# Optimization experiments

Hardware: AMD Instinct MI355X
Metric: run time of the kernel (lower is better)

## Reference

```python
import jax, jax.numpy as jnp
import numpy as np

HIDDEN = 2048
INTER = 5632
N_EXPERTS = 8
TOP_K = 2


def setup_inputs() -> dict:
    key = jax.random.key(0)
    ks = jax.random.split(key, 6)
    x = jax.random.normal(ks[0], (4, 2048, HIDDEN), dtype=jnp.float32)
    router_w = jax.random.normal(ks[1], (N_EXPERTS, HIDDEN), dtype=jnp.float32) * 0.02
    router_b = jnp.zeros((N_EXPERTS,), dtype=jnp.float32)
    Wg = jax.random.normal(ks[2], (N_EXPERTS, INTER, HIDDEN), dtype=jnp.float32) * 0.02
    Wu = jax.random.normal(ks[3], (N_EXPERTS, INTER, HIDDEN), dtype=jnp.float32) * 0.02
    Wd = jax.random.normal(ks[4], (N_EXPERTS, HIDDEN, INTER), dtype=jnp.float32) * 0.02
    return {"x": x, "router_w": router_w, "router_b": router_b, "Wg": Wg, "Wu": Wu, "Wd": Wd}


def reference(x, router_w, router_b, Wg, Wu, Wd):
    batch_shape = x.shape[:-1]
    xf = x.reshape(-1, HIDDEN)  # [T, H]
    T = xf.shape[0]

    # Router: softmax -> top-k -> renormalize (matches torch forward)
    logits = xf @ router_w.T + router_b            # [T, E]
    probs = jax.nn.softmax(logits, axis=-1)
    w, idx = jax.lax.top_k(probs, TOP_K)           # [T, K]
    w = w / jnp.sum(w, axis=-1, keepdims=True)

    # Dense combine weights [T, E]: zero where expert not selected.
    combine = jnp.zeros((T, N_EXPERTS), dtype=xf.dtype)
    combine = combine.at[jnp.arange(T)[:, None], idx].set(w)

    # Weighted sum of SwiGLU expert outputs (loop over fixed small E).
    out = jnp.zeros_like(xf)
    for e in range(N_EXPERTS):
        g = jax.nn.silu(xf @ Wg[e].T)              # [T, I]
        u = xf @ Wu[e].T                           # [T, I]
        h = (g * u) @ Wd[e].T                      # [T, H]
        out = out + combine[:, e:e + 1] * h
    return out.reshape(*batch_shape, HIDDEN)
```

## Files before the change

kernel.cpp:

```cpp
#include <hip/hip_runtime.h>
#include <stdint.h>

#define HID 2048
#define ITR 5632
#define NE 8
#define TT 8192
#define BM 128
#define BN 128
#define BK 64
#define MT1 64
#define NT1 44
#define NT2 16

typedef __attribute__((ext_vector_type(4))) float f4;
typedef __attribute__((ext_vector_type(8))) short s8v;
typedef __attribute__((ext_vector_type(4))) float acc4;
typedef __attribute__((ext_vector_type(4))) unsigned short u4v;
typedef __attribute__((ext_vector_type(8))) unsigned short u8v;

__device__ __forceinline__ unsigned short f2bf(float f) {
    union { float f; uint32_t u; } v; v.f = f;
    uint32_t u = v.u;
    return (unsigned short)((u + 0x7FFFu + ((u >> 16) & 1u)) >> 16);
}

__device__ __forceinline__ void gload16(const unsigned short* g, unsigned short* l) {
    __builtin_amdgcn_global_load_lds(
        (const __attribute__((address_space(1))) unsigned int*)g,
        (__attribute__((address_space(3))) unsigned int*)l, 16, 0, 0);
}

__global__ __launch_bounds__(256) void k_cvt(const float* __restrict__ src,
                                             unsigned short* __restrict__ dst) {
    size_t i = ((size_t)blockIdx.x * 256 + threadIdx.x) * 8;
    f4 a = *(const f4*)(src + i);
    f4 b = *(const f4*)(src + i + 4);
    u8v o;
    o[0]=f2bf(a.x); o[1]=f2bf(a.y); o[2]=f2bf(a.z); o[3]=f2bf(a.w);
    o[4]=f2bf(b.x); o[5]=f2bf(b.y); o[6]=f2bf(b.z); o[7]=f2bf(b.w);
    *(u8v*)(dst + i) = o;
}

#define WBLK 45056
__global__ __launch_bounds__(256) void k_cvtW(const float* __restrict__ a,
                                              const float* __restrict__ b,
                                              const float* __restrict__ c,
                                              unsigned short* __restrict__ oa,
                                              unsigned short* __restrict__ ob,
                                              unsigned short* __restrict__ oc) {
    int bb = blockIdx.x;
    const float* s; unsigned short* d;
    if (bb < WBLK)            { s = a; d = oa; }
    else if (bb < 2 * WBLK)   { s = b; d = ob; bb -= WBLK; }
    else                      { s = c; d = oc; bb -= 2 * WBLK; }
    size_t i = ((size_t)bb * 256 + threadIdx.x) * 8;
    f4 va = *(const f4*)(s + i);
    f4 vb = *(const f4*)(s + i + 4);
    u8v o;
    o[0]=f2bf(va.x); o[1]=f2bf(va.y); o[2]=f2bf(va.z); o[3]=f2bf(va.w);
    o[4]=f2bf(vb.x); o[5]=f2bf(vb.y); o[6]=f2bf(vb.z); o[7]=f2bf(vb.w);
    *(u8v*)(d + i) = o;
}

__global__ __launch_bounds__(256) void k_router(const float* __restrict__ x,
                                                const float* __restrict__ rw,
                                                const float* __restrict__ rb,
                                                int* __restrict__ cnt,
                                                int* __restrict__ tokL,
                                                int* __restrict__ slotL,
                                                float* __restrict__ gateL) {
    int lane = threadIdx.x & 63;
    int wv = threadIdx.x >> 6;
    int t = blockIdx.x * 4 + wv;
    const float* xr = x + (size_t)t * HID;
    float acc[NE];
    #pragma unroll
    for (int e = 0; e < NE; ++e) acc[e] = 0.f;
    #pragma unroll
    for (int i = 0; i < 8; ++i) {
        f4 xv = *(const f4*)(xr + i * 256 + lane * 4);
        #pragma unroll
        for (int e = 0; e < NE; ++e) {
            f4 wv4 = *(const f4*)(rw + e * HID + i * 256 + lane * 4);
            acc[e] += xv.x * wv4.x + xv.y * wv4.y + xv.z * wv4.z + xv.w * wv4.w;
        }
    }
    #pragma unroll
    for (int off = 32; off; off >>= 1)
        #pragma unroll
        for (int e = 0; e < NE; ++e) acc[e] += __shfl_xor(acc[e], off, 64);
    if (lane == 0) {
        float lg[NE];
        #pragma unroll
        for (int e = 0; e < NE; ++e) lg[e] = acc[e] + rb[e];
        int i1 = 0;
        #pragma unroll
        for (int e = 1; e < NE; ++e) if (lg[e] > lg[i1]) i1 = e;
        int i2 = -1;
        #pragma unroll
        for (int e = 0; e < NE; ++e) {
            if (e == i1) continue;
            if (i2 < 0 || lg[e] > lg[i2]) i2 = e;
        }
        float ex = __expf(lg[i2] - lg[i1]);
        float w1 = 1.f / (1.f + ex);
        float w2 = ex / (1.f + ex);
        int p = atomicAdd(&cnt[i1], 1);
        tokL[i1 * TT + p] = t; slotL[i1 * TT + p] = t * 2;     gateL[i1 * TT + p] = w1;
        p = atomicAdd(&cnt[i2], 1);
        tokL[i2 * TT + p] = t; slotL[i2 * TT + p] = t * 2 + 1; gateL[i2 * TT + p] = w2;
    }
}


__global__ __launch_bounds__(256, 2) void k_gemm1b(const unsigned short* __restrict__ xb,
                                                   const unsigned short* __restrict__ WgB,
                                                   const unsigned short* __restrict__ WuB,
                                                   const int* __restrict__ cnt,
                                                   const int* __restrict__ tokL,
                                                   const int* __restrict__ slotL,
                                                   unsigned short* __restrict__ Hb) {
    int bx = blockIdx.x;
    int xcd = bx & 7;
    int j = bx >> 3;
    int g = xcd * NT1 + (j >> 6);
    int mt = j & 63;
    int e = g / NT1;
    int nt = g % NT1;
    int M = cnt[e];
    int m0 = mt * BM;
    if (m0 >= M) return;
    int n0 = nt * BN;

    __shared__ __align__(16) unsigned short lA[BM * BK];
    __shared__ __align__(16) unsigned short lBg[BN * BK];
    __shared__ __align__(16) unsigned short lBu[BN * BK];
    __shared__ int sTok[BM];
    __shared__ int sSlot[BM];

    int tid = threadIdx.x;
    if (tid < BM) {
        int m = m0 + tid;
        int mc = m < M ? m : M - 1;
        sTok[tid] = tokL[e * TT + mc];
        sSlot[tid] = slotL[e * TT + mc];
    }
    __syncthreads();

    int wv = tid >> 6, lane = tid & 63;
    int subrow = lane >> 3;
    int colE = ((lane & 7) ^ subrow) * 8;

    const unsigned short* aSrc[4];
    const unsigned short* gSrc[4];
    const unsigned short* uSrc[4];
    #pragma unroll
    for (int i = 0; i < 4; ++i) {
        int row = (i * 4 + wv) * 8 + subrow;
        aSrc[i] = xb + (size_t)sTok[row] * HID + colE;
        gSrc[i] = WgB + ((size_t)e * ITR + n0 + row) * HID + colE;
        uSrc[i] = WuB + ((size_t)e * ITR + n0 + row) * HID + colE;
    }

    int wm = (wv >> 1) * 64, wn = (wv & 1) * 64;
    int lr = lane & 15, lk = (lane >> 4) * 8;

    acc4 zero4 = {0.f, 0.f, 0.f, 0.f};
    acc4 ag[4][4], au[4][4];
    #pragma unroll
    for (int mi = 0; mi < 4; ++mi)
        #pragma unroll
        for (int ni = 0; ni < 4; ++ni) { ag[mi][ni] = zero4; au[mi][ni] = zero4; }

    for (int k0 = 0; k0 < HID; k0 += BK) {
        if (k0) __syncthreads();
        #pragma unroll
        for (int i = 0; i < 4; ++i) {
            gload16(aSrc[i] + k0, lA  + (i * 4 + wv) * 512);
            gload16(gSrc[i] + k0, lBg + (i * 4 + wv) * 512);
            gload16(uSrc[i] + k0, lBu + (i * 4 + wv) * 512);
        }
        __syncthreads();
        #pragma unroll
        for (int kk = 0; kk < BK; kk += 32) {
            s8v af[4], gf[4], uf[4];
            #pragma unroll
            for (int i = 0; i < 4; ++i) {
                int rowA = wm + i * 16 + lr;
                af[i] = *(const s8v*)((char*)lA + ((rowA * 128 + (kk + lk) * 2) ^ ((rowA & 7) << 4)));
                int rowB = wn + i * 16 + lr;
                int bb = (rowB * 128 + (kk + lk) * 2) ^ ((rowB & 7) << 4);
                gf[i] = *(const s8v*)((char*)lBg + bb);
                uf[i] = *(const s8v*)((char*)lBu + bb);
            }
            #pragma unroll
            for (int mi = 0; mi < 4; ++mi)
                #pragma unroll
                for (int ni = 0; ni < 4; ++ni) {
                    ag[mi][ni] = __builtin_amdgcn_mfma_f32_16x16x32_bf16(af[mi], gf[ni], ag[mi][ni], 0, 0, 0);
                    au[mi][ni] = __builtin_amdgcn_mfma_f32_16x16x32_bf16(af[mi], uf[ni], au[mi][ni], 0, 0, 0);
                }
        }
    }
    #pragma unroll
    for (int mi = 0; mi < 4; ++mi) {
        #pragma unroll
        for (int j2 = 0; j2 < 4; ++j2) {
            int m = wm + mi * 16 + (lane >> 4) * 4 + j2;
            if (m0 + m < M) {
                size_t rowOff = (size_t)sSlot[m] * ITR + n0 + wn + lr;
                #pragma unroll
                for (int ni = 0; ni < 4; ++ni) {
                    float g2 = ag[mi][ni][j2], u = au[mi][ni][j2];
                    float h = g2 * (1.f / (1.f + __expf(-g2))) * u;
                    Hb[rowOff + ni * 16] = f2bf(h);
                }
            }
        }
    }
}

__global__ __launch_bounds__(256, 3) void k_gemm2b(const unsigned short* __restrict__ Hb,
                                                   const unsigned short* __restrict__ WdB,
                                                   const int* __restrict__ cnt,
                                                   const int* __restrict__ tokL,
                                                   const int* __restrict__ slotL,
                                                   const float* __restrict__ gateL,
                                                   float* __restrict__ out) {
    int bx = blockIdx.x;
    int xcd = bx & 7;
    int j = bx >> 3;
    int g = xcd * NT2 + (j >> 6);
    int mt = j & 63;
    int e = g / NT2;
    int nt = g % NT2;
    int M = cnt[e];
    int m0 = mt * BM;
    if (m0 >= M) return;
    int n0 = nt * BN;

    __shared__ __align__(16) unsigned short lA[BM * BK];
    __shared__ __align__(16) unsigned short lB[BN * BK];
    __shared__ int sTok[BM];
    __shared__ int sSlot[BM];
    __shared__ float sGate[BM];

    int tid = threadIdx.x;
    if (tid < BM) {
        int m = m0 + tid;
        int mc = m < M ? m : M - 1;
        sTok[tid] = tokL[e * TT + mc];
        sSlot[tid] = slotL[e * TT + mc];
        sGate[tid] = gateL[e * TT + mc];
    }
    __syncthreads();

    int wv = tid >> 6, lane = tid & 63;
    int subrow = lane >> 3;
    int colE = ((lane & 7) ^ subrow) * 8;

    const unsigned short* aSrc[4];
    const unsigned short* bSrc[4];
    #pragma unroll
    for (int i = 0; i < 4; ++i) {
        int row = (i * 4 + wv) * 8 + subrow;
        aSrc[i] = Hb + (size_t)sSlot[row] * ITR + colE;
        bSrc[i] = WdB + ((size_t)e * HID + n0 + row) * ITR + colE;
    }

    int wm = (wv >> 1) * 64, wn = (wv & 1) * 64;
    int lr = lane & 15, lk = (lane >> 4) * 8;

    acc4 zero4 = {0.f, 0.f, 0.f, 0.f};
    acc4 a4[4][4];
    #pragma unroll
    for (int mi = 0; mi < 4; ++mi)
        #pragma unroll
        for (int ni = 0; ni < 4; ++ni) a4[mi][ni] = zero4;

    for (int k0 = 0; k0 < ITR; k0 += BK) {
        if (k0) __syncthreads();
        #pragma unroll
        for (int i = 0; i < 4; ++i) {
            gload16(aSrc[i] + k0, lA + (i * 4 + wv) * 512);
            gload16(bSrc[i] + k0, lB + (i * 4 + wv) * 512);
        }
        __syncthreads();
        #pragma unroll
        for (int kk = 0; kk < BK; kk += 32) {
            s8v af[4], bf[4];
            #pragma unroll
            for (int i = 0; i < 4; ++i) {
                int rowA = wm + i * 16 + lr;
                af[i] = *(const s8v*)((char*)lA + ((rowA * 128 + (kk + lk) * 2) ^ ((rowA & 7) << 4)));
                int rowB = wn + i * 16 + lr;
                bf[i] = *(const s8v*)((char*)lB + ((rowB * 128 + (kk + lk) * 2) ^ ((rowB & 7) << 4)));
            }
            #pragma unroll
            for (int mi = 0; mi < 4; ++mi)
                #pragma unroll
                for (int ni = 0; ni < 4; ++ni)
                    a4[mi][ni] = __builtin_amdgcn_mfma_f32_16x16x32_bf16(af[mi], bf[ni], a4[mi][ni], 0, 0, 0);
        }
    }
    #pragma unroll
    for (int mi = 0; mi < 4; ++mi) {
        #pragma unroll
        for (int j2 = 0; j2 < 4; ++j2) {
            int m = wm + mi * 16 + (lane >> 4) * 4 + j2;
            if (m0 + m < M) {
                int t = sTok[m];
                float w = sGate[m];
                float* orow = out + (size_t)t * HID + n0 + wn + lr;
                #pragma unroll
                for (int ni = 0; ni < 4; ++ni)
                    atomicAdd(orow + ni * 16, w * a4[mi][ni][j2]);
            }
        }
    }
}


__global__ __launch_bounds__(256) void k_gemm1(const unsigned short* __restrict__ xb,
                                               const float* __restrict__ Wg,
                                               const float* __restrict__ Wu,
                                               const int* __restrict__ cnt,
                                               const int* __restrict__ tokL,
                                               const int* __restrict__ slotL,
                                               unsigned short* __restrict__ Hb) {
    int bx = blockIdx.x;
    int e = bx / (MT1 * NT1);
    int r = bx % (MT1 * NT1);
    int mt = r / NT1, nt = r % NT1;
    int M = cnt[e];
    int m0 = mt * BM;
    if (m0 >= M) return;
    int n0 = nt * BN;

    __shared__ __align__(16) unsigned short lA[BM * BK];
    __shared__ __align__(16) unsigned short lBg[BN * BK];
    __shared__ __align__(16) unsigned short lBu[BN * BK];
    __shared__ int sTok[BM];
    __shared__ int sSlot[BM];

    int tid = threadIdx.x;
    if (tid < BM) {
        int m = m0 + tid;
        int mc = m < M ? m : M - 1;
        sTok[tid] = tokL[e * TT + mc];
        sSlot[tid] = slotL[e * TT + mc];
    }
    __syncthreads();

    int ar = tid >> 3, ac = tid & 7;
    const unsigned short* aP[4];
    #pragma unroll
    for (int i = 0; i < 4; ++i)
        aP[i] = xb + (size_t)sTok[ar + 32 * i] * HID + ac * 8;

    int br = tid >> 4, bc = tid & 15;
    const float* gB = Wg + ((size_t)e * ITR + n0) * HID + bc * 4;
    const float* uB = Wu + ((size_t)e * ITR + n0) * HID + bc * 4;

    int wv = tid >> 6, lane = tid & 63;
    int wm = (wv >> 1) * 64, wn = (wv & 1) * 64;
    int lr = lane & 15, lk = (lane >> 4) * 8;

    acc4 zero4 = {0.f, 0.f, 0.f, 0.f};
    acc4 ag[4][4], au[4][4];
    #pragma unroll
    for (int mi = 0; mi < 4; ++mi)
        #pragma unroll
        for (int ni = 0; ni < 4; ++ni) { ag[mi][ni] = zero4; au[mi][ni] = zero4; }

    for (int k0 = 0; k0 < HID; k0 += BK) {
        if (k0) __syncthreads();
        #pragma unroll
        for (int i = 0; i < 4; ++i) {
            int row = ar + 32 * i;
            s8v v = *(const s8v*)(aP[i] + k0);
            int byt = (row * 128 + ac * 16) ^ ((row & 7) << 4);
            *(s8v*)((char*)lA + byt) = v;
        }
        #pragma unroll
        for (int i = 0; i < 8; ++i) {
            int row = br + 16 * i;
            f4 vg = *(const f4*)(gB + (size_t)row * HID + k0);
            f4 vu = *(const f4*)(uB + (size_t)row * HID + k0);
            u4v og = { f2bf(vg.x), f2bf(vg.y), f2bf(vg.z), f2bf(vg.w) };
            u4v ou = { f2bf(vu.x), f2bf(vu.y), f2bf(vu.z), f2bf(vu.w) };
            int byt = (row * 128 + bc * 8) ^ ((row & 7) << 4);
            *(u4v*)((char*)lBg + byt) = og;
            *(u4v*)((char*)lBu + byt) = ou;
        }
        __syncthreads();
        #pragma unroll
        for (int kk = 0; kk < BK; kk += 32) {
            s8v af[4], gf[4], uf[4];
            #pragma unroll
            for (int i = 0; i < 4; ++i) {
                int rowA = wm + i * 16 + lr;
                af[i] = *(const s8v*)((char*)lA + ((rowA * 128 + (kk + lk) * 2) ^ ((rowA & 7) << 4)));
                int rowB = wn + i * 16 + lr;
                int bb = (rowB * 128 + (kk + lk) * 2) ^ ((rowB & 7) << 4);
                gf[i] = *(const s8v*)((char*)lBg + bb);
                uf[i] = *(const s8v*)((char*)lBu + bb);
            }
            #pragma unroll
            for (int mi = 0; mi < 4; ++mi)
                #pragma unroll
                for (int ni = 0; ni < 4; ++ni) {
                    ag[mi][ni] = __builtin_amdgcn_mfma_f32_16x16x32_bf16(af[mi], gf[ni], ag[mi][ni], 0, 0, 0);
                    au[mi][ni] = __builtin_amdgcn_mfma_f32_16x16x32_bf16(af[mi], uf[ni], au[mi][ni], 0, 0, 0);
                }
        }
    }
    #pragma unroll
    for (int mi = 0; mi < 4; ++mi) {
        #pragma unroll
        for (int j = 0; j < 4; ++j) {
            int m = wm + mi * 16 + (lane >> 4) * 4 + j;
            if (m0 + m < M) {
                size_t rowOff = (size_t)sSlot[m] * ITR + n0 + wn + lr;
                #pragma unroll
                for (int ni = 0; ni < 4; ++ni) {
                    float g = ag[mi][ni][j], u = au[mi][ni][j];
                    float h = g * (1.f / (1.f + __expf(-g))) * u;
                    Hb[rowOff + ni * 16] = f2bf(h);
                }
            }
        }
    }
}

__global__ __launch_bounds__(256) void k_gemm2(const unsigned short* __restrict__ Hb,
                                               const float* __restrict__ Wd,
                                               const int* __restrict__ cnt,
                                               const int* __restrict__ tokL,
                                               const int* __restrict__ slotL,
                                               const float* __restrict__ gateL,
                                               float* __restrict__ out) {
    int bx = blockIdx.x;
    int e = bx / (MT1 * NT2);
    int r = bx % (MT1 * NT2);
    int mt = r / NT2, nt = r % NT2;
    int M = cnt[e];
    int m0 = mt * BM;
    if (m0 >= M) return;
    int n0 = nt * BN;

    __shared__ __align__(16) unsigned short lA[BM * BK];
    __shared__ __align__(16) unsigned short lB[BN * BK];
    __shared__ int sTok[BM];
    __shared__ int sSlot[BM];
    __shared__ float sGate[BM];

    int tid = threadIdx.x;
    if (tid < BM) {
        int m = m0 + tid;
        int mc = m < M ? m : M - 1;
        sTok[tid] = tokL[e * TT + mc];
        sSlot[tid] = slotL[e * TT + mc];
        sGate[tid] = gateL[e * TT + mc];
    }
    __syncthreads();

    int ar = tid >> 3, ac = tid & 7;
    const unsigned short* aP[4];
    #pragma unroll
    for (int i = 0; i < 4; ++i)
        aP[i] = Hb + (size_t)sSlot[ar + 32 * i] * ITR + ac * 8;

    int br = tid >> 4, bc = tid & 15;
    const float* dB = Wd + ((size_t)e * HID + n0) * ITR + bc * 4;

    int wv = tid >> 6, lane = tid & 63;
    int wm = (wv >> 1) * 64, wn = (wv & 1) * 64;
    int lr = lane & 15, lk = (lane >> 4) * 8;

    acc4 zero4 = {0.f, 0.f, 0.f, 0.f};
    acc4 a4[4][4];
    #pragma unroll
    for (int mi = 0; mi < 4; ++mi)
        #pragma unroll
        for (int ni = 0; ni < 4; ++ni) a4[mi][ni] = zero4;

    for (int k0 = 0; k0 < ITR; k0 += BK) {
        if (k0) __syncthreads();
        #pragma unroll
        for (int i = 0; i < 4; ++i) {
            int row = ar + 32 * i;
            s8v v = *(const s8v*)(aP[i] + k0);
            int byt = (row * 128 + ac * 16) ^ ((row & 7) << 4);
            *(s8v*)((char*)lA + byt) = v;
        }
        #pragma unroll
        for (int i = 0; i < 8; ++i) {
            int row = br + 16 * i;
            f4 vd = *(const f4*)(dB + (size_t)row * ITR + k0);
            u4v od = { f2bf(vd.x), f2bf(vd.y), f2bf(vd.z), f2bf(vd.w) };
            int byt = (row * 128 + bc * 8) ^ ((row & 7) << 4);
            *(u4v*)((char*)lB + byt) = od;
        }
        __syncthreads();
        #pragma unroll
        for (int kk = 0; kk < BK; kk += 32) {
            s8v af[4], bf[4];
            #pragma unroll
            for (int i = 0; i < 4; ++i) {
                int rowA = wm + i * 16 + lr;
                af[i] = *(const s8v*)((char*)lA + ((rowA * 128 + (kk + lk) * 2) ^ ((rowA & 7) << 4)));
                int rowB = wn + i * 16 + lr;
                bf[i] = *(const s8v*)((char*)lB + ((rowB * 128 + (kk + lk) * 2) ^ ((rowB & 7) << 4)));
            }
            #pragma unroll
            for (int mi = 0; mi < 4; ++mi)
                #pragma unroll
                for (int ni = 0; ni < 4; ++ni)
                    a4[mi][ni] = __builtin_amdgcn_mfma_f32_16x16x32_bf16(af[mi], bf[ni], a4[mi][ni], 0, 0, 0);
        }
    }
    #pragma unroll
    for (int mi = 0; mi < 4; ++mi) {
        #pragma unroll
        for (int j = 0; j < 4; ++j) {
            int m = wm + mi * 16 + (lane >> 4) * 4 + j;
            if (m0 + m < M) {
                int t = sTok[m];
                float w = sGate[m];
                float* orow = out + (size_t)t * HID + n0 + wn + lr;
                #pragma unroll
                for (int ni = 0; ni < 4; ++ni)
                    atomicAdd(orow + ni * 16, w * a4[mi][ni][j]);
            }
        }
    }
}

extern "C" void kernel_launch(void* const* d_in, const int* in_sizes, int n_in,
                              void* d_out, int out_size, void* d_ws, size_t ws_size,
                              hipStream_t stream) {
    const float* x  = (const float*)d_in[0];
    const float* rw = (const float*)d_in[1];
    const float* rb = (const float*)d_in[2];
    const float* Wg = (const float*)d_in[3];
    const float* Wu = (const float*)d_in[4];
    const float* Wd = (const float*)d_in[5];
    float* out = (float*)d_out;
    char* ws = (char*)d_ws;

    const size_t OFF_XB   = 0;
    const size_t OFF_HB   = 33554432ull;
    const size_t OFF_TOK  = 218103808ull;
    const size_t OFF_SLOT = 218365952ull;
    const size_t OFF_GATE = 218628096ull;
    const size_t OFF_CNT  = 218890240ull;
    const size_t OFF_WG   = 218891264ull;
    const size_t OFF_WU   = 403440640ull;
    const size_t OFF_WD   = 587990016ull;
    const size_t NEED     = 772539392ull;

    unsigned short* xb   = (unsigned short*)(ws + OFF_XB);
    unsigned short* Hb   = (unsigned short*)(ws + OFF_HB);
    int*   tokL  = (int*)(ws + OFF_TOK);
    int*   slotL = (int*)(ws + OFF_SLOT);
    float* gateL = (float*)(ws + OFF_GATE);
    int*   cnt   = (int*)(ws + OFF_CNT);

    hipMemsetAsync(cnt, 0, NE * sizeof(int), stream);
    hipMemsetAsync(out, 0, (size_t)out_size * sizeof(float), stream);
    k_cvt<<<8192, 256, 0, stream>>>(x, xb);
    k_router<<<2048, 256, 0, stream>>>(x, rw, rb, cnt, tokL, slotL, gateL);

    if (ws_size >= NEED) {
        unsigned short* WgB = (unsigned short*)(ws + OFF_WG);
        unsigned short* WuB = (unsigned short*)(ws + OFF_WU);
        unsigned short* WdB = (unsigned short*)(ws + OFF_WD);
        k_cvtW<<<3 * WBLK, 256, 0, stream>>>(Wg, Wu, Wd, WgB, WuB, WdB);
        k_gemm1b<<<NE * MT1 * NT1, 256, 0, stream>>>(xb, WgB, WuB, cnt, tokL, slotL, Hb);
        k_gemm2b<<<NE * MT1 * NT2, 256, 0, stream>>>(Hb, WdB, cnt, tokL, slotL, gateL, out);
    } else {
        k_gemm1<<<NE * MT1 * NT1, 256, 0, stream>>>(xb, Wg, Wu, cnt, tokL, slotL, Hb);
        k_gemm2<<<NE * MT1 * NT2, 256, 0, stream>>>(Hb, Wd, cnt, tokL, slotL, gateL, out);
    }
}
```

Measured before the change: 1.909 ms.

## Replace grouped GEMM kernels with 512-thread, 4-stage pipelined, larger-tile versions

Replaces both expert GEMM kernels with 512-thread variants that use 256-row tiles and a 4-deep ring of 32-wide K slices in LDS. Direct global-to-LDS loads for later stages are issued while MFMAs run on the current stage, with manual waitcnt/barrier control and raised priority around the MFMA block. The larger tiles raise reuse of weight and activation loads, and the ring buffer hides global latency behind compute. The trade-off is higher LDS use and register pressure. The XCD-aware block remapping is also dropped, and expert-row imbalance may leave more 256-row tiles partly empty.

```diff
diff --git a/kernel.cpp b/kernel.cpp
--- a/kernel.cpp
+++ b/kernel.cpp
@@ -5,18 +5,13 @@
 #define ITR 5632
 #define NE 8
 #define TT 8192
-#define BM 128
-#define BN 128
-#define BK 64
-#define MT1 64
-#define NT1 44
-#define NT2 16
 
 typedef __attribute__((ext_vector_type(4))) float f4;
 typedef __attribute__((ext_vector_type(8))) short s8v;
 typedef __attribute__((ext_vector_type(4))) float acc4;
 typedef __attribute__((ext_vector_type(4))) unsigned short u4v;
 typedef __attribute__((ext_vector_type(8))) unsigned short u8v;
+typedef unsigned short ushort_t;
 
 __device__ __forceinline__ unsigned short f2bf(float f) {
     union { float f; uint32_t u; } v; v.f = f;
@@ -28,6 +23,10 @@
     __builtin_amdgcn_global_load_lds(
         (const __attribute__((address_space(1))) unsigned int*)g,
         (__attribute__((address_space(3))) unsigned int*)l, 16, 0, 0);
+}
+
+__device__ __forceinline__ int lby(int row, int s) {
+    return row * 64 + ((s ^ ((row >> 1) & 3)) * 16);
 }
 
 __global__ __launch_bounds__(256) void k_cvt(const float* __restrict__ src,
@@ -113,20 +112,263 @@
 }
 
 
-__global__ __launch_bounds__(256, 2) void k_gemm1b(const unsigned short* __restrict__ xb,
-                                                   const unsigned short* __restrict__ WgB,
-                                                   const unsigned short* __restrict__ WuB,
-                                                   const int* __restrict__ cnt,
-                                                   const int* __restrict__ tokL,
-                                                   const int* __restrict__ slotL,
-                                                   unsigned short* __restrict__ Hb) {
+__global__ __launch_bounds__(512, 2) void k_g1p(const unsigned short* __restrict__ xb,
+                                                const unsigned short* __restrict__ WgB,
+                                                const unsigned short* __restrict__ WuB,
+                                                const int* __restrict__ cnt,
+                                                const int* __restrict__ tokL,
+                                                const int* __restrict__ slotL,
+                                                unsigned short* __restrict__ Hb) {
     int bx = blockIdx.x;
-    int xcd = bx & 7;
-    int j = bx >> 3;
-    int g = xcd * NT1 + (j >> 6);
-    int mt = j & 63;
-    int e = g / NT1;
-    int nt = g % NT1;
+    int e = bx / (32 * 44);
+    int r = bx % (32 * 44);
+    int mt = r / 44, nt = r % 44;
+    int M = cnt[e];
+    int m0 = mt * 256;
+    if (m0 >= M) return;
+    int n0 = nt * 128;
+
+    __shared__ __align__(16) unsigned short lds[65536];
+    __shared__ int sTok[256];
+    __shared__ int sSlot[256];
+
+    int tid = threadIdx.x;
+    if (tid < 256) {
+        int m = m0 + tid;
+        int mc = m < M ? m : M - 1;
+        sTok[tid]  = tokL[e * TT + mc];
+        sSlot[tid] = slotL[e * TT + mc];
+    }
+    __syncthreads();
+
+    int wv = tid >> 6, lane = tid & 63;
+    int lrow = lane >> 2;
+    int slog = (lane & 3) ^ ((lane >> 3) & 3);
+
+    const unsigned short* aS0 = xb + (size_t)sTok[(2 * wv) * 16 + lrow] * HID + slog * 8;
+    const unsigned short* aS1 = xb + (size_t)sTok[(2 * wv + 1) * 16 + lrow] * HID + slog * 8;
+    const unsigned short* gS  = WgB + ((size_t)e * ITR + n0 + wv * 16 + lrow) * HID + slog * 8;
+    const unsigned short* uS  = WuB + ((size_t)e * ITR + n0 + wv * 16 + lrow) * HID + slog * 8;
+
+    unsigned short* ldsA = lds;
+    unsigned short* ldsG = lds + 32768;
+    unsigned short* ldsU = lds + 49152;
+
+    auto STAGE = [&](int reg, int kh) {
+        int ko = kh * 32;
+        gload16(aS0 + ko, ldsA + reg * 8192 + (2 * wv) * 512);
+        gload16(aS1 + ko, ldsA + reg * 8192 + (2 * wv + 1) * 512);
+        gload16(gS + ko,  ldsG + reg * 4096 + wv * 512);
+        gload16(uS + ko,  ldsU + reg * 4096 + wv * 512);
+    };
+
+    int wr = wv >> 2, wc = wv & 3;
+    int lr = lane & 15, ls = lane >> 4;
+
+    int aOff[8], gOff[2], uOff[2];
+    #pragma unroll
+    for (int mi = 0; mi < 8; ++mi) aOff[mi] = lby(wr * 128 + mi * 16 + lr, ls);
+    #pragma unroll
+    for (int ni = 0; ni < 2; ++ni) {
+        gOff[ni] = 65536 + lby(wc * 32 + ni * 16 + lr, ls);
+        uOff[ni] = 98304 + lby(wc * 32 + ni * 16 + lr, ls);
+    }
+
+    acc4 zero4 = {0.f, 0.f, 0.f, 0.f};
+    acc4 ag[8][2], au[8][2];
+    #pragma unroll
+    for (int mi = 0; mi < 8; ++mi)
+        #pragma unroll
+        for (int ni = 0; ni < 2; ++ni) { ag[mi][ni] = zero4; au[mi][ni] = zero4; }
+
+    STAGE(0, 0); STAGE(1, 1); STAGE(2, 2); STAGE(3, 3);
+    asm volatile("s_waitcnt vmcnt(12)" ::: "memory");
+    __builtin_amdgcn_s_barrier();
+
+    #pragma unroll 4
+    for (int h = 0; h < 64; ++h) {
+        int reg = h & 3;
+        const char* baseA = (const char*)lds + reg * 16384;
+        const char* baseB = (const char*)lds + reg * 8192;
+        s8v af[8], gf[2], uf[2];
+        #pragma unroll
+        for (int mi = 0; mi < 8; ++mi) af[mi] = *(const s8v*)(baseA + aOff[mi]);
+        #pragma unroll
+        for (int ni = 0; ni < 2; ++ni) {
+            gf[ni] = *(const s8v*)(baseB + gOff[ni]);
+            uf[ni] = *(const s8v*)(baseB + uOff[ni]);
+        }
+        asm volatile("s_waitcnt lgkmcnt(0)" ::: "memory");
+        __builtin_amdgcn_sched_barrier(0);
+        __builtin_amdgcn_s_barrier();
+        __builtin_amdgcn_sched_barrier(0);
+        int kh = h + 4 < 64 ? h + 4 : 63;
+        STAGE(reg, kh);
+        __builtin_amdgcn_s_setprio(1);
+        #pragma unroll
+        for (int mi = 0; mi < 8; ++mi)
+            #pragma unroll
+            for (int ni = 0; ni < 2; ++ni) {
+                ag[mi][ni] = __builtin_amdgcn_mfma_f32_16x16x32_bf16(af[mi], gf[ni], ag[mi][ni], 0, 0, 0);
+                au[mi][ni] = __builtin_amdgcn_mfma_f32_16x16x32_bf16(af[mi], uf[ni], au[mi][ni], 0, 0, 0);
+            }
+        __builtin_amdgcn_s_setprio(0);
+        asm volatile("s_waitcnt vmcnt(12)" ::: "memory");
+        __builtin_amdgcn_s_barrier();
+    }
+    asm volatile("s_waitcnt vmcnt(0)" ::: "memory");
+
+    #pragma unroll
+    for (int mi = 0; mi < 8; ++mi) {
+        #pragma unroll
+        for (int j = 0; j < 4; ++j) {
+            int m = wr * 128 + mi * 16 + ls * 4 + j;
+            if (m0 + m < M) {
+                size_t rowOff = (size_t)sSlot[m] * ITR + n0 + wc * 32 + lr;
+                #pragma unroll
+                for (int ni = 0; ni < 2; ++ni) {
+                    float g = ag[mi][ni][j], u = au[mi][ni][j];
+                    float h2 = g * (1.f / (1.f + __expf(-g))) * u;
+                    Hb[rowOff + ni * 16] = f2bf(h2);
+                }
+            }
+        }
+    }
+}
+
+__global__ __launch_bounds__(512, 2) void k_g2p(const unsigned short* __restrict__ Hb,
+                                                const unsigned short* __restrict__ WdB,
+                                                const int* __restrict__ cnt,
+                                                const int* __restrict__ tokL,
+                                                const int* __restrict__ slotL,
+                                                const float* __restrict__ gateL,
+                                                float* __restrict__ out) {
+    int bx = blockIdx.x;
+    int e = bx / (32 * 8);
+    int r = bx % (32 * 8);
+    int mt = r / 8, nt = r % 8;
+    int M = cnt[e];
+    int m0 = mt * 256;
+    if (m0 >= M) return;
+    int n0 = nt * 256;
+
+    __shared__ __align__(16) unsigned short lds[65536];
+    __shared__ int sTok[256];
+    __shared__ int sSlot[256];
+    __shared__ float sGate[256];
+
+    int tid = threadIdx.x;
+    if (tid < 256) {
+        int m = m0 + tid;
+        int mc = m < M ? m : M - 1;
+        sTok[tid]  = tokL[e * TT + mc];
+        sSlot[tid] = slotL[e * TT + mc];
+        sGate[tid] = gateL[e * TT + mc];
+    }
+    __syncthreads();
+
+    int wv = tid >> 6, lane = tid & 63;
+    int lrow = lane >> 2;
+    int slog = (lane & 3) ^ ((lane >> 3) & 3);
+
+    const unsigned short* aS0 = Hb + (size_t)sSlot[(2 * wv) * 16 + lrow] * ITR + slog * 8;
+    const unsigned short* aS1 = Hb + (size_t)sSlot[(2 * wv + 1) * 16 + lrow] * ITR + slog * 8;
+    const unsigned short* bS0 = WdB + ((size_t)e * HID + n0 + (2 * wv) * 16 + lrow) * ITR + slog * 8;
+    const unsigned short* bS1 = WdB + ((size_t)e * HID + n0 + (2 * wv + 1) * 16 + lrow) * ITR + slog * 8;
+
+    unsigned short* ldsA = lds;
+    unsigned short* ldsB = lds + 32768;
+
+    auto STAGE = [&](int reg, int kh) {
+        int ko = kh * 32;
+        gload16(aS0 + ko, ldsA + reg * 8192 + (2 * wv) * 512);
+        gload16(aS1 + ko, ldsA + reg * 8192 + (2 * wv + 1) * 512);
+        gload16(bS0 + ko, ldsB + reg * 8192 + (2 * wv) * 512);
+        gload16(bS1 + ko, ldsB + reg * 8192 + (2 * wv + 1) * 512);
+    };
+
+    int wr = wv >> 2, wc = wv & 3;
+    int lr = lane & 15, ls = lane >> 4;
+
+    int aOff[8], bOff[4];
+    #pragma unroll
+    for (int mi = 0; mi < 8; ++mi) aOff[mi] = lby(wr * 128 + mi * 16 + lr, ls);
+    #pragma unroll
+    for (int ni = 0; ni < 4; ++ni) bOff[ni] = 65536 + lby(wc * 64 + ni * 16 + lr, ls);
+
+    acc4 zero4 = {0.f, 0.f, 0.f, 0.f};
+    acc4 a4[8][4];
+    #pragma unroll
+    for (int mi = 0; mi < 8; ++mi)
+        #pragma unroll
+        for (int ni = 0; ni < 4; ++ni) a4[mi][ni] = zero4;
+
+    STAGE(0, 0); STAGE(1, 1); STAGE(2, 2); STAGE(3, 3);
+    asm volatile("s_waitcnt vmcnt(12)" ::: "memory");
+    __builtin_amdgcn_s_barrier();
+
+    #pragma unroll 4
+    for (int h = 0; h < 176; ++h) {
+        int reg = h & 3;
+        const char* base = (const char*)lds + reg * 16384;
+        s8v af[8], bf[4];
+        #pragma unroll
+        for (int mi = 0; mi < 8; ++mi) af[mi] = *(const s8v*)(base + aOff[mi]);
+        #pragma unroll
+        for (int ni = 0; ni < 4; ++ni) bf[ni] = *(const s8v*)(base + bOff[ni]);
+        asm volatile("s_waitcnt lgkmcnt(0)" ::: "memory");
+        __builtin_amdgcn_sched_barrier(0);
+        __builtin_amdgcn_s_barrier();
+        __builtin_amdgcn_sched_barrier(0);
+        int kh = h + 4 < 176 ? h + 4 : 175;
+        STAGE(reg, kh);
+        __builtin_amdgcn_s_setprio(1);
+        #pragma unroll
+        for (int mi = 0; mi < 8; ++mi)
+            #pragma unroll
+            for (int ni = 0; ni < 4; ++ni)
+                a4[mi][ni] = __builtin_amdgcn_mfma_f32_16x16x32_bf16(af[mi], bf[ni], a4[mi][ni], 0, 0, 0);
+        __builtin_amdgcn_s_setprio(0);
+        asm volatile("s_waitcnt vmcnt(12)" ::: "memory");
+        __builtin_amdgcn_s_barrier();
+    }
+    asm volatile("s_waitcnt vmcnt(0)" ::: "memory");
+
+    #pragma unroll
+    for (int mi = 0; mi < 8; ++mi) {
+        #pragma unroll
+        for (int j = 0; j < 4; ++j) {
+            int m = wr * 128 + mi * 16 + ls * 4 + j;
+            if (m0 + m < M) {
+                int t = sTok[m];
+                float w = sGate[m];
+                float* orow = out + (size_t)t * HID + n0 + wc * 64 + lr;
+                #pragma unroll
+                for (int ni = 0; ni < 4; ++ni)
+                    atomicAdd(orow + ni * 16, w * a4[mi][ni][j]);
+            }
+        }
+    }
+}
+
+#define BM 128
+#define BN 128
+#define BK 64
+#define MT1 64
+#define NT1 44
+#define NT2 16
+
+__global__ __launch_bounds__(256) void k_gemm1(const unsigned short* __restrict__ xb,
+                                               const float* __restrict__ Wg,
+                                               const float* __restrict__ Wu,
+                                               const int* __restrict__ cnt,
+                                               const int* __restrict__ tokL,
+                                               const int* __restrict__ slotL,
+                                               unsigned short* __restrict__ Hb) {
+    int bx = blockIdx.x;
+    int e = bx / (MT1 * NT1);
+    int r = bx % (MT1 * NT1);
+    int mt = r / NT1, nt = r % NT1;
     int M = cnt[e];
     int m0 = mt * BM;
     if (m0 >= M) return;
@@ -147,21 +389,17 @@
     }
     __syncthreads();
 
+    int ar = tid >> 3, ac = tid & 7;
+    const unsigned short* aP[4];
+    #pragma unroll
+    for (int i = 0; i < 4; ++i)
+        aP[i] = xb + (size_t)sTok[ar + 32 * i] * HID + ac * 8;
+
+    int br = tid >> 4, bc = tid & 15;
+    const float* gB = Wg + ((size_t)e * ITR + n0) * HID + bc * 4;
+    const float* uB = Wu + ((size_t)e * ITR + n0) * HID + bc * 4;
+
     int wv = tid >> 6, lane = tid & 63;
-    int subrow = lane >> 3;
-    int colE = ((lane & 7) ^ subrow) * 8;
-
-    const unsigned short* aSrc[4];
-    const unsigned short* gSrc[4];
-    const unsigned short* uSrc[4];
-    #pragma unroll
-    for (int i = 0; i < 4; ++i) {
-        int row = (i * 4 + wv) * 8 + subrow;
-        aSrc[i] = xb + (size_t)sTok[row] * HID + colE;
-        gSrc[i] = WgB + ((size_t)e * ITR + n0 + row) * HID + colE;
-        uSrc[i] = WuB + ((size_t)e * ITR + n0 + row) * HID + colE;
-    }
-
     int wm = (wv >> 1) * 64, wn = (wv & 1) * 64;
     int lr = lane & 15, lk = (lane >> 4) * 8;
 
@@ -176,9 +414,21 @@
         if (k0) __syncthreads();
         #pragma unroll
         for (int i = 0; i < 4; ++i) {
-            gload16(aSrc[i] + k0, lA  + (i * 4 + wv) * 512);
-            gload16(gSrc[i] + k0, lBg + (i * 4 + wv) * 512);
-            gload16(uSrc[i] + k0, lBu + (i * 4 + wv) * 512);
+            int row = ar + 32 * i;
+            s8v v = *(const s8v*)(aP[i] + k0);
+            int byt = (row * 128 + ac * 16) ^ ((row & 7) << 4);
+            *(s8v*)((char*)lA + byt) = v;
+        }
+        #pragma unroll
+        for (int i = 0; i < 8; ++i) {
+            int row = br + 16 * i;
+            f4 vg = *(const f4*)(gB + (size_t)row * HID + k0);
+            f4 vu = *(const f4*)(uB + (size_t)row * HID + k0);
+            u4v og = { f2bf(vg.x), f2bf(vg.y), f2bf(vg.z), f2bf(vg.w) };
+            u4v ou = { f2bf(vu.x), f2bf(vu.y), f2bf(vu.z), f2bf(vu.w) };
+            int byt = (row * 128 + bc * 8) ^ ((row & 7) << 4);
+            *(u4v*)((char*)lBg + byt) = og;
+            *(u4v*)((char*)lBu + byt) = ou;
         }
         __syncthreads();
         #pragma unroll
@@ -205,219 +455,6 @@
     #pragma unroll
     for (int mi = 0; mi < 4; ++mi) {
         #pragma unroll
-        for (int j2 = 0; j2 < 4; ++j2) {
-            int m = wm + mi * 16 + (lane >> 4) * 4 + j2;
-            if (m0 + m < M) {
-                size_t rowOff = (size_t)sSlot[m] * ITR + n0 + wn + lr;
-                #pragma unroll
-                for (int ni = 0; ni < 4; ++ni) {
-                    float g2 = ag[mi][ni][j2], u = au[mi][ni][j2];
-                    float h = g2 * (1.f / (1.f + __expf(-g2))) * u;
-                    Hb[rowOff + ni * 16] = f2bf(h);
-                }
-            }
-        }
-    }
-}
-
-__global__ __launch_bounds__(256, 3) void k_gemm2b(const unsigned short* __restrict__ Hb,
-                                                   const unsigned short* __restrict__ WdB,
-                                                   const int* __restrict__ cnt,
-                                                   const int* __restrict__ tokL,
-                                                   const int* __restrict__ slotL,
-                                                   const float* __restrict__ gateL,
-                                                   float* __restrict__ out) {
-    int bx = blockIdx.x;
-    int xcd = bx & 7;
-    int j = bx >> 3;
-    int g = xcd * NT2 + (j >> 6);
-    int mt = j & 63;
-    int e = g / NT2;
-    int nt = g % NT2;
-    int M = cnt[e];
-    int m0 = mt * BM;
-    if (m0 >= M) return;
-    int n0 = nt * BN;
-
-    __shared__ __align__(16) unsigned short lA[BM * BK];
-    __shared__ __align__(16) unsigned short lB[BN * BK];
-    __shared__ int sTok[BM];
-    __shared__ int sSlot[BM];
-    __shared__ float sGate[BM];
-
-    int tid = threadIdx.x;
-    if (tid < BM) {
-        int m = m0 + tid;
-        int mc = m < M ? m : M - 1;
-        sTok[tid] = tokL[e * TT + mc];
-        sSlot[tid] = slotL[e * TT + mc];
-        sGate[tid] = gateL[e * TT + mc];
-    }
-    __syncthreads();
-
-    int wv = tid >> 6, lane = tid & 63;
-    int subrow = lane >> 3;
-    int colE = ((lane & 7) ^ subrow) * 8;
-
-    const unsigned short* aSrc[4];
-    const unsigned short* bSrc[4];
-    #pragma unroll
-    for (int i = 0; i < 4; ++i) {
-        int row = (i * 4 + wv) * 8 + subrow;
-        aSrc[i] = Hb + (size_t)sSlot[row] * ITR + colE;
-        bSrc[i] = WdB + ((size_t)e * HID + n0 + row) * ITR + colE;
-    }
-
-    int wm = (wv >> 1) * 64, wn = (wv & 1) * 64;
-    int lr = lane & 15, lk = (lane >> 4) * 8;
-
-    acc4 zero4 = {0.f, 0.f, 0.f, 0.f};
-    acc4 a4[4][4];
-    #pragma unroll
-    for (int mi = 0; mi < 4; ++mi)
-        #pragma unroll
-        for (int ni = 0; ni < 4; ++ni) a4[mi][ni] = zero4;
-
-    for (int k0 = 0; k0 < ITR; k0 += BK) {
-        if (k0) __syncthreads();
-        #pragma unroll
-        for (int i = 0; i < 4; ++i) {
-            gload16(aSrc[i] + k0, lA + (i * 4 + wv) * 512);
-            gload16(bSrc[i] + k0, lB + (i * 4 + wv) * 512);
-        }
-        __syncthreads();
-        #pragma unroll
-        for (int kk = 0; kk < BK; kk += 32) {
-            s8v af[4], bf[4];
-            #pragma unroll
-            for (int i = 0; i < 4; ++i) {
-                int rowA = wm + i * 16 + lr;
-                af[i] = *(const s8v*)((char*)lA + ((rowA * 128 + (kk + lk) * 2) ^ ((rowA & 7) << 4)));
-                int rowB = wn + i * 16 + lr;
-                bf[i] = *(const s8v*)((char*)lB + ((rowB * 128 + (kk + lk) * 2) ^ ((rowB & 7) << 4)));
-            }
-            #pragma unroll
-            for (int mi = 0; mi < 4; ++mi)
-                #pragma unroll
-                for (int ni = 0; ni < 4; ++ni)
-                    a4[mi][ni] = __builtin_amdgcn_mfma_f32_16x16x32_bf16(af[mi], bf[ni], a4[mi][ni], 0, 0, 0);
-        }
-    }
-    #pragma unroll
-    for (int mi = 0; mi < 4; ++mi) {
-        #pragma unroll
-        for (int j2 = 0; j2 < 4; ++j2) {
-            int m = wm + mi * 16 + (lane >> 4) * 4 + j2;
-            if (m0 + m < M) {
-                int t = sTok[m];
-                float w = sGate[m];
-                float* orow = out + (size_t)t * HID + n0 + wn + lr;
-                #pragma unroll
-                for (int ni = 0; ni < 4; ++ni)
-                    atomicAdd(orow + ni * 16, w * a4[mi][ni][j2]);
-            }
-        }
-    }
-}
-
-
-__global__ __launch_bounds__(256) void k_gemm1(const unsigned short* __restrict__ xb,
-                                               const float* __restrict__ Wg,
-                                               const float* __restrict__ Wu,
-                                               const int* __restrict__ cnt,
-                                               const int* __restrict__ tokL,
-                                               const int* __restrict__ slotL,
-                                               unsigned short* __restrict__ Hb) {
-    int bx = blockIdx.x;
-    int e = bx / (MT1 * NT1);
-    int r = bx % (MT1 * NT1);
-    int mt = r / NT1, nt = r % NT1;
-    int M = cnt[e];
-    int m0 = mt * BM;
-    if (m0 >= M) return;
-    int n0 = nt * BN;
-
-    __shared__ __align__(16) unsigned short lA[BM * BK];
-    __shared__ __align__(16) unsigned short lBg[BN * BK];
-    __shared__ __align__(16) unsigned short lBu[BN * BK];
-    __shared__ int sTok[BM];
-    __shared__ int sSlot[BM];
-
-    int tid = threadIdx.x;
-    if (tid < BM) {
-        int m = m0 + tid;
-        int mc = m < M ? m : M - 1;
-        sTok[tid] = tokL[e * TT + mc];
-        sSlot[tid] = slotL[e * TT + mc];
-    }
-    __syncthreads();
-
-    int ar = tid >> 3, ac = tid & 7;
-    const unsigned short* aP[4];
-    #pragma unroll
-    for (int i = 0; i < 4; ++i)
-        aP[i] = xb + (size_t)sTok[ar + 32 * i] * HID + ac * 8;
-
-    int br = tid >> 4, bc = tid & 15;
-    const float* gB = Wg + ((size_t)e * ITR + n0) * HID + bc * 4;
-    const float* uB = Wu + ((size_t)e * ITR + n0) * HID + bc * 4;
-
-    int wv = tid >> 6, lane = tid & 63;
-    int wm = (wv >> 1) * 64, wn = (wv & 1) * 64;
-    int lr = lane & 15, lk = (lane >> 4) * 8;
-
-    acc4 zero4 = {0.f, 0.f, 0.f, 0.f};
-    acc4 ag[4][4], au[4][4];
-    #pragma unroll
-    for (int mi = 0; mi < 4; ++mi)
-        #pragma unroll
-        for (int ni = 0; ni < 4; ++ni) { ag[mi][ni] = zero4; au[mi][ni] = zero4; }
-
-    for (int k0 = 0; k0 < HID; k0 += BK) {
-        if (k0) __syncthreads();
-        #pragma unroll
-        for (int i = 0; i < 4; ++i) {
-            int row = ar + 32 * i;
-            s8v v = *(const s8v*)(aP[i] + k0);
-            int byt = (row * 128 + ac * 16) ^ ((row & 7) << 4);
-            *(s8v*)((char*)lA + byt) = v;
-        }
-        #pragma unroll
-        for (int i = 0; i < 8; ++i) {
-            int row = br + 16 * i;
-            f4 vg = *(const f4*)(gB + (size_t)row * HID + k0);
-            f4 vu = *(const f4*)(uB + (size_t)row * HID + k0);
-            u4v og = { f2bf(vg.x), f2bf(vg.y), f2bf(vg.z), f2bf(vg.w) };
-            u4v ou = { f2bf(vu.x), f2bf(vu.y), f2bf(vu.z), f2bf(vu.w) };
-            int byt = (row * 128 + bc * 8) ^ ((row & 7) << 4);
-            *(u4v*)((char*)lBg + byt) = og;
-            *(u4v*)((char*)lBu + byt) = ou;
-        }
-        __syncthreads();
-        #pragma unroll
-        for (int kk = 0; kk < BK; kk += 32) {
-            s8v af[4], gf[4], uf[4];
-            #pragma unroll
-            for (int i = 0; i < 4; ++i) {
-                int rowA = wm + i * 16 + lr;
-                af[i] = *(const s8v*)((char*)lA + ((rowA * 128 + (kk + lk) * 2) ^ ((rowA & 7) << 4)));
-                int rowB = wn + i * 16 + lr;
-                int bb = (rowB * 128 + (kk + lk) * 2) ^ ((rowB & 7) << 4);
-                gf[i] = *(const s8v*)((char*)lBg + bb);
-                uf[i] = *(const s8v*)((char*)lBu + bb);
-            }
-            #pragma unroll
-            for (int mi = 0; mi < 4; ++mi)
-                #pragma unroll
-                for (int ni = 0; ni < 4; ++ni) {
-                    ag[mi][ni] = __builtin_amdgcn_mfma_f32_16x16x32_bf16(af[mi], gf[ni], ag[mi][ni], 0, 0, 0);
-                    au[mi][ni] = __builtin_amdgcn_mfma_f32_16x16x32_bf16(af[mi], uf[ni], au[mi][ni], 0, 0, 0);
-                }
-        }
-    }
-    #pragma unroll
-    for (int mi = 0; mi < 4; ++mi) {
-        #pragma unroll
         for (int j = 0; j < 4; ++j) {
             int m = wm + mi * 16 + (lane >> 4) * 4 + j;
             if (m0 + m < M) {
@@ -577,8 +614,8 @@
         unsigned short* WuB = (unsigned short*)(ws + OFF_WU);
         unsigned short* WdB = (unsigned short*)(ws + OFF_WD);
         k_cvtW<<<3 * WBLK, 256, 0, stream>>>(Wg, Wu, Wd, WgB, WuB, WdB);
-        k_gemm1b<<<NE * MT1 * NT1, 256, 0, stream>>>(xb, WgB, WuB, cnt, tokL, slotL, Hb);
-        k_gemm2b<<<NE * MT1 * NT2, 256, 0, stream>>>(Hb, WdB, cnt, tokL, slotL, gateL, out);
+        k_g1p<<<NE * 32 * 44, 512, 0, stream>>>(xb, WgB, WuB, cnt, tokL, slotL, Hb);
+        k_g2p<<<NE * 32 * 8, 512, 0, stream>>>(Hb, WdB, cnt, tokL, slotL, gateL, out);
     } else {
         k_gemm1<<<NE * MT1 * NT1, 256, 0, stream>>>(xb, Wg, Wu, cnt, tokL, slotL, Hb);
         k_gemm2<<<NE * MT1 * NT2, 256, 0, stream>>>(Hb, Wd, cnt, tokL, slotL, gateL, out);
```

Result: no change. 1.938 ms (+1.5%).

## Fuse x bf16 conversion into router and drop XCD block swizzle

Applied to the files above, without the earlier changes.

Merges the standalone fp32-to-bf16 conversion of x into the router kernel, so x is read once and one launch is removed. Also replaces the XCD-aware block index remapping in both expert GEMMs with a plain linear expert/m-tile/n-tile decomposition. The fusion cuts memory traffic. Dropping the swizzle risks worse L2 locality, because blocks sharing weight tiles now spread across chiplets.

```diff
diff --git a/kernel.cpp b/kernel.cpp
--- a/kernel.cpp
+++ b/kernel.cpp
@@ -30,15 +30,60 @@
         (__attribute__((address_space(3))) unsigned int*)l, 16, 0, 0);
 }
 
-__global__ __launch_bounds__(256) void k_cvt(const float* __restrict__ src,
-                                             unsigned short* __restrict__ dst) {
-    size_t i = ((size_t)blockIdx.x * 256 + threadIdx.x) * 8;
-    f4 a = *(const f4*)(src + i);
-    f4 b = *(const f4*)(src + i + 4);
-    u8v o;
-    o[0]=f2bf(a.x); o[1]=f2bf(a.y); o[2]=f2bf(a.z); o[3]=f2bf(a.w);
-    o[4]=f2bf(b.x); o[5]=f2bf(b.y); o[6]=f2bf(b.z); o[7]=f2bf(b.w);
-    *(u8v*)(dst + i) = o;
+#define MFMA16(a, b, c) __builtin_amdgcn_mfma_f32_16x16x32_bf16(a, b, c, 0, 0, 0)
+
+__global__ __launch_bounds__(256) void k_xrt(const float* __restrict__ x,
+                                             const float* __restrict__ rw,
+                                             const float* __restrict__ rb,
+                                             unsigned short* __restrict__ xb,
+                                             int* __restrict__ cnt,
+                                             int* __restrict__ tokL,
+                                             int* __restrict__ slotL,
+                                             float* __restrict__ gateL) {
+    int lane = threadIdx.x & 63;
+    int wv = threadIdx.x >> 6;
+    int t = blockIdx.x * 4 + wv;
+    const float* xr = x + (size_t)t * HID;
+    unsigned short* xo = xb + (size_t)t * HID;
+    float acc[NE];
+    #pragma unroll
+    for (int e = 0; e < NE; ++e) acc[e] = 0.f;
+    #pragma unroll
+    for (int i = 0; i < 8; ++i) {
+        f4 xv = *(const f4*)(xr + i * 256 + lane * 4);
+        u4v o = { f2bf(xv.x), f2bf(xv.y), f2bf(xv.z), f2bf(xv.w) };
+        *(u4v*)(xo + i * 256 + lane * 4) = o;
+        #pragma unroll
+        for (int e = 0; e < NE; ++e) {
+            f4 wv4 = *(const f4*)(rw + e * HID + i * 256 + lane * 4);
+            acc[e] += xv.x * wv4.x + xv.y * wv4.y + xv.z * wv4.z + xv.w * wv4.w;
+        }
+    }
+    #pragma unroll
+    for (int off = 32; off; off >>= 1)
+        #pragma unroll
+        for (int e = 0; e < NE; ++e) acc[e] += __shfl_xor(acc[e], off, 64);
+    if (lane == 0) {
+        float lg[NE];
+        #pragma unroll
+        for (int e = 0; e < NE; ++e) lg[e] = acc[e] + rb[e];
+        int i1 = 0;
+        #pragma unroll
+        for (int e = 1; e < NE; ++e) if (lg[e] > lg[i1]) i1 = e;
+        int i2 = -1;
+        #pragma unroll
+        for (int e = 0; e < NE; ++e) {
+            if (e == i1) continue;
+            if (i2 < 0 || lg[e] > lg[i2]) i2 = e;
+        }
+        float ex = __expf(lg[i2] - lg[i1]);
+        float w1 = 1.f / (1.f + ex);
+        float w2 = ex / (1.f + ex);
+        int p = atomicAdd(&cnt[i1], 1);
+        tokL[i1 * TT + p] = t; slotL[i1 * TT + p] = t * 2;     gateL[i1 * TT + p] = w1;
+        p = atomicAdd(&cnt[i2], 1);
+        tokL[i2 * TT + p] = t; slotL[i2 * TT + p] = t * 2 + 1; gateL[i2 * TT + p] = w2;
+    }
 }
 
 #define WBLK 45056
@@ -62,54 +107,15 @@
     *(u8v*)(d + i) = o;
 }
 
-__global__ __launch_bounds__(256) void k_router(const float* __restrict__ x,
-                                                const float* __restrict__ rw,
-                                                const float* __restrict__ rb,
-                                                int* __restrict__ cnt,
-                                                int* __restrict__ tokL,
-                                                int* __restrict__ slotL,
-                                                float* __restrict__ gateL) {
-    int lane = threadIdx.x & 63;
-    int wv = threadIdx.x >> 6;
-    int t = blockIdx.x * 4 + wv;
-    const float* xr = x + (size_t)t * HID;
-    float acc[NE];
-    #pragma unroll
-    for (int e = 0; e < NE; ++e) acc[e] = 0.f;
-    #pragma unroll
-    for (int i = 0; i < 8; ++i) {
-        f4 xv = *(const f4*)(xr + i * 256 + lane * 4);
-        #pragma unroll
-        for (int e = 0; e < NE; ++e) {
-            f4 wv4 = *(const f4*)(rw + e * HID + i * 256 + lane * 4);
-            acc[e] += xv.x * wv4.x + xv.y * wv4.y + xv.z * wv4.z + xv.w * wv4.w;
-        }
-    }
-    #pragma unroll
-    for (int off = 32; off; off >>= 1)
-        #pragma unroll
-        for (int e = 0; e < NE; ++e) acc[e] += __shfl_xor(acc[e], off, 64);
-    if (lane == 0) {
-        float lg[NE];
-        #pragma unroll
-        for (int e = 0; e < NE; ++e) lg[e] = acc[e] + rb[e];
-        int i1 = 0;
-        #pragma unroll
-        for (int e = 1; e < NE; ++e) if (lg[e] > lg[i1]) i1 = e;
-        int i2 = -1;
-        #pragma unroll
-        for (int e = 0; e < NE; ++e) {
-            if (e == i1) continue;
-            if (i2 < 0 || lg[e] > lg[i2]) i2 = e;
-        }
-        float ex = __expf(lg[i2] - lg[i1]);
-        float w1 = 1.f / (1.f + ex);
-        float w2 = ex / (1.f + ex);
-        int p = atomicAdd(&cnt[i1], 1);
-        tokL[i1 * TT + p] = t; slotL[i1 * TT + p] = t * 2;     gateL[i1 * TT + p] = w1;
-        p = atomicAdd(&cnt[i2], 1);
-        tokL[i2 * TT + p] = t; slotL[i2 * TT + p] = t * 2 + 1; gateL[i2 * TT + p] = w2;
-    }
+__global__ __launch_bounds__(256) void k_cvt(const float* __restrict__ src,
+                                             unsigned short* __restrict__ dst) {
+    size_t i = ((size_t)blockIdx.x * 256 + threadIdx.x) * 8;
+    f4 a = *(const f4*)(src + i);
+    f4 b = *(const f4*)(src + i + 4);
+    u8v o;
+    o[0]=f2bf(a.x); o[1]=f2bf(a.y); o[2]=f2bf(a.z); o[3]=f2bf(a.w);
+    o[4]=f2bf(b.x); o[5]=f2bf(b.y); o[6]=f2bf(b.z); o[7]=f2bf(b.w);
+    *(u8v*)(dst + i) = o;
 }
 
 
@@ -121,12 +127,9 @@
                                                    const int* __restrict__ slotL,
                                                    unsigned short* __restrict__ Hb) {
     int bx = blockIdx.x;
-    int xcd = bx & 7;
-    int j = bx >> 3;
-    int g = xcd * NT1 + (j >> 6);
-    int mt = j & 63;
-    int e = g / NT1;
-    int nt = g % NT1;
+    int e = bx / (MT1 * NT1);
+    int r = bx % (MT1 * NT1);
+    int mt = r / NT1, nt = r % NT1;
     int M = cnt[e];
     int m0 = mt * BM;
     if (m0 >= M) return;
@@ -197,8 +200,8 @@
             for (int mi = 0; mi < 4; ++mi)
                 #pragma unroll
                 for (int ni = 0; ni < 4; ++ni) {
-                    ag[mi][ni] = __builtin_amdgcn_mfma_f32_16x16x32_bf16(af[mi], gf[ni], ag[mi][ni], 0, 0, 0);
-                    au[mi][ni] = __builtin_amdgcn_mfma_f32_16x16x32_bf16(af[mi], uf[ni], au[mi][ni], 0, 0, 0);
+                    ag[mi][ni] = MFMA16(af[mi], gf[ni], ag[mi][ni]);
+                    au[mi][ni] = MFMA16(af[mi], uf[ni], au[mi][ni]);
                 }
         }
     }
@@ -211,8 +214,8 @@
                 size_t rowOff = (size_t)sSlot[m] * ITR + n0 + wn + lr;
                 #pragma unroll
                 for (int ni = 0; ni < 4; ++ni) {
-                    float g2 = ag[mi][ni][j2], u = au[mi][ni][j2];
-                    float h = g2 * (1.f / (1.f + __expf(-g2))) * u;
+                    float g = ag[mi][ni][j2], u = au[mi][ni][j2];
+                    float h = g * (1.f / (1.f + __expf(-g))) * u;
                     Hb[rowOff + ni * 16] = f2bf(h);
                 }
             }
@@ -228,12 +231,9 @@
                                                    const float* __restrict__ gateL,
                                                    float* __restrict__ out) {
     int bx = blockIdx.x;
-    int xcd = bx & 7;
-    int j = bx >> 3;
-    int g = xcd * NT2 + (j >> 6);
-    int mt = j & 63;
-    int e = g / NT2;
-    int nt = g % NT2;
+    int e = bx / (MT1 * NT2);
+    int r = bx % (MT1 * NT2);
+    int mt = r / NT2, nt = r % NT2;
     int M = cnt[e];
     int m0 = mt * BM;
     if (m0 >= M) return;
@@ -300,7 +300,7 @@
             for (int mi = 0; mi < 4; ++mi)
                 #pragma unroll
                 for (int ni = 0; ni < 4; ++ni)
-                    a4[mi][ni] = __builtin_amdgcn_mfma_f32_16x16x32_bf16(af[mi], bf[ni], a4[mi][ni], 0, 0, 0);
+                    a4[mi][ni] = MFMA16(af[mi], bf[ni], a4[mi][ni]);
         }
     }
     #pragma unroll
@@ -410,8 +410,8 @@
             for (int mi = 0; mi < 4; ++mi)
                 #pragma unroll
                 for (int ni = 0; ni < 4; ++ni) {
-                    ag[mi][ni] = __builtin_amdgcn_mfma_f32_16x16x32_bf16(af[mi], gf[ni], ag[mi][ni], 0, 0, 0);
-                    au[mi][ni] = __builtin_amdgcn_mfma_f32_16x16x32_bf16(af[mi], uf[ni], au[mi][ni], 0, 0, 0);
+                    ag[mi][ni] = MFMA16(af[mi], gf[ni], ag[mi][ni]);
+                    au[mi][ni] = MFMA16(af[mi], uf[ni], au[mi][ni]);
                 }
         }
     }
@@ -517,7 +517,7 @@
             for (int mi = 0; mi < 4; ++mi)
                 #pragma unroll
                 for (int ni = 0; ni < 4; ++ni)
-                    a4[mi][ni] = __builtin_amdgcn_mfma_f32_16x16x32_bf16(af[mi], bf[ni], a4[mi][ni], 0, 0, 0);
+                    a4[mi][ni] = MFMA16(af[mi], bf[ni], a4[mi][ni]);
         }
     }
     #pragma unroll
@@ -569,8 +569,7 @@
 
     hipMemsetAsync(cnt, 0, NE * sizeof(int), stream);
     hipMemsetAsync(out, 0, (size_t)out_size * sizeof(float), stream);
-    k_cvt<<<8192, 256, 0, stream>>>(x, xb);
-    k_router<<<2048, 256, 0, stream>>>(x, rw, rb, cnt, tokL, slotL, gateL);
+    k_xrt<<<2048, 256, 0, stream>>>(x, rw, rb, xb, cnt, tokL, slotL, gateL);
 
     if (ws_size >= NEED) {
         unsigned short* WgB = (unsigned short*)(ws + OFF_WG);
```

New measurement: 1.806 ms. 1.06x faster.
